# Performance work log

Measured on AMD Instinct MI355X. Metric: run time of the kernel, lower is better.

Reference implementation:

```python
import jax, jax.numpy as jnp
import numpy as np

B, S, D_MODEL, H, D_HEAD = 4, 2048, 1024, 16, 64
SCALE = D_HEAD ** -0.5


def setup_inputs() -> dict:
    key = jax.random.key(0)
    ks = jax.random.split(key, 6)
    init = lambda k, shp: jax.random.normal(k, shp, jnp.float32) * (shp[0] ** -0.5)
    Xq = jax.random.normal(ks[0], (B, S, D_MODEL), jnp.float32)
    # pre-softmax bool mask: True = masked (fill -inf) -> causal
    mask_bef = jnp.triu(jnp.ones((S, S), dtype=bool), k=1)
    # post-softmax bool mask: True = zero out that attention weight
    mask_aft = jax.random.bernoulli(ks[1], 0.1, (S, S))
    Wq = init(ks[2], (D_MODEL, H * D_HEAD))
    Wk = init(ks[3], (D_MODEL, H * D_HEAD))
    Wv = init(ks[4], (D_MODEL, H * D_HEAD))
    Wo = init(ks[5], (H * D_HEAD, D_MODEL))
    return {"Xq": Xq, "mask_bef": mask_bef, "mask_aft": mask_aft,
            "Wq": Wq, "Wk": Wk, "Wv": Wv, "Wo": Wo}


def reference(Xq, mask_bef, mask_aft, Wq, Wk, Wv, Wo):
    # Self-attention: Xk = Xv = Xq
    def split_heads(X, W):  # [B,S,D] @ [D,H*d] -> [B,H,S,d]
        return (X @ W).reshape(B, S, H, D_HEAD).transpose(0, 2, 1, 3)

    Q = split_heads(Xq, Wq)
    K = split_heads(Xq, Wk)
    V = split_heads(Xq, Wv)
    # scores: [B,H,Sq,Sk]
    scores = jnp.einsum('bhqd,bhkd->bhqk', Q, K) * SCALE
    scores = jnp.where(mask_bef, -jnp.inf, scores)  # pre-softmax bool mask
    attn = jax.nn.softmax(scores, axis=-1)
    attn = jnp.where(mask_aft, 0.0, attn)           # post-softmax bool mask
    out = jnp.einsum('bhqk,bhkd->bhqd', attn, V)    # [B,H,S,d]
    out = out.transpose(0, 2, 1, 3).reshape(B, S, H * D_HEAD)
    return out @ Wo  # [B,S,out_dim_o]
```

## Files before the change

### kernel.cpp

```cpp
#include <hip/hip_runtime.h>
#include <hip/hip_bf16.h>


using bf16 = __hip_bfloat16;
typedef __attribute__((ext_vector_type(8))) short short8;
typedef __attribute__((ext_vector_type(4))) float floatx4;

#define kB 4
#define kS 2048
#define kDM 1024
#define kH 16
#define kDH 64
#define kHeadElems ((size_t)kB * kH * kS * kDH)
#define STR 72

__device__ __forceinline__ float bfu(unsigned short v) {
    return __uint_as_float(((unsigned)v) << 16);
}
__device__ __forceinline__ unsigned short f2bf(float f) {
    union { float f; unsigned u; } x{f};
    unsigned r = x.u + 0x7fff + ((x.u >> 16) & 1);
    return (unsigned short)(r >> 16);
}
__device__ __forceinline__ void gl_lds16(const void* g, void* l) {
    __builtin_amdgcn_global_load_lds(
        (const __attribute__((address_space(1))) unsigned int*)g,
        (__attribute__((address_space(3))) unsigned int*)l, 16, 0, 0);
}

__global__ __launch_bounds__(256)
void pack_mask(const int* __restrict__ mask_aft, unsigned long long* __restrict__ mp)
{
    const int widx = blockIdx.x * 4 + (threadIdx.x >> 6);
    const int lane = threadIdx.x & 63;
    const int q = widx >> 5, w64 = widx & 31;
    const int key = w64 * 64 + lane;
    const int m = mask_aft[(size_t)q * kS + key];
    const unsigned long long b = __ballot(m != 0 || key > q);
    if (lane == 0) mp[widx] = b;
}

__global__ __launch_bounds__(256)
void conv_x(const float* __restrict__ X, bf16* __restrict__ Xb)
{
    const size_t i = ((size_t)blockIdx.x * 256 + threadIdx.x) * 8;
    const float4 a = *(const float4*)(X + i);
    const float4 b = *(const float4*)(X + i + 4);
    union { unsigned short u[8]; uint4 v; } o;
    o.u[0] = f2bf(a.x); o.u[1] = f2bf(a.y); o.u[2] = f2bf(a.z); o.u[3] = f2bf(a.w);
    o.u[4] = f2bf(b.x); o.u[5] = f2bf(b.y); o.u[6] = f2bf(b.z); o.u[7] = f2bf(b.w);
    *(uint4*)(Xb + i) = o.v;
}

__global__ __launch_bounds__(256)
void conv_wT(const float* __restrict__ W, bf16* __restrict__ WT)
{
    __shared__ unsigned short Ls[64][STR];
    const int k0 = blockIdx.x * 64, n0 = blockIdx.y * 64;
    const int tid = threadIdx.x;
    const int r16 = tid >> 4, c4 = (tid & 15) * 4;
    #pragma unroll
    for (int it = 0; it < 4; ++it) {
        const int r = it * 16 + r16;
        const float4 v = *(const float4*)(W + (size_t)(k0 + r) * kDM + n0 + c4);
        Ls[c4 + 0][r] = f2bf(v.x); Ls[c4 + 1][r] = f2bf(v.y);
        Ls[c4 + 2][r] = f2bf(v.z); Ls[c4 + 3][r] = f2bf(v.w);
    }
    __syncthreads();
    #pragma unroll
    for (int it = 0; it < 4; ++it) {
        const int rn = it * 16 + r16;
        ushort4 u;
        u.x = Ls[rn][c4 + 0]; u.y = Ls[rn][c4 + 1];
        u.z = Ls[rn][c4 + 2]; u.w = Ls[rn][c4 + 3];
        *(ushort4*)(WT + (size_t)(n0 + rn) * kDM + k0 + c4) = u;
    }
}

__global__ __launch_bounds__(256)
void qkv_mfma(const bf16* __restrict__ A, const bf16* __restrict__ BT,
              bf16* __restrict__ ws)
{
    __shared__ __align__(16) unsigned short At[128][32];
    __shared__ __align__(16) unsigned short Bt[128][32];
    const int tid = threadIdx.x;
    const int w = tid >> 6, lane = tid & 63;
    const int quad = (tid >> 4) & 3, col = tid & 15;
    const int wm = w >> 1, wn = w & 1;
    const int n0 = blockIdx.x * 128;
    const int m0 = blockIdx.y * 128;

    const bf16* pA = A  + (size_t)(m0 + w * 32 + (lane >> 2)) * kDM + (lane & 3) * 8;
    const bf16* pB = BT + (size_t)(n0 + w * 32 + (lane >> 2)) * kDM + (lane & 3) * 8;
    unsigned short* lA = &At[w * 32][0];
    unsigned short* lB = &Bt[w * 32][0];

    floatx4 acc[4][4];
    #pragma unroll
    for (int i = 0; i < 4; ++i)
        #pragma unroll
        for (int j = 0; j < 4; ++j) acc[i][j] = (floatx4){0.f, 0.f, 0.f, 0.f};

    for (int k0 = 0; k0 < kDM; k0 += 32) {
        __syncthreads();
        gl_lds16(pA + k0, lA);
        gl_lds16(pA + k0 + 16 * kDM, lA + 16 * 32);
        gl_lds16(pB + k0, lB);
        gl_lds16(pB + k0 + 16 * kDM, lB + 16 * 32);
        __syncthreads();
        short8 aA[4], bB[4];
        #pragma unroll
        for (int i = 0; i < 4; ++i)
            aA[i] = *(const short8*)&At[wm * 64 + i * 16 + col][quad * 8];
        #pragma unroll
        for (int j = 0; j < 4; ++j)
            bB[j] = *(const short8*)&Bt[wn * 64 + j * 16 + col][quad * 8];
        #pragma unroll
        for (int i = 0; i < 4; ++i)
            #pragma unroll
            for (int j = 0; j < 4; ++j)
                acc[i][j] = __builtin_amdgcn_mfma_f32_16x16x32_bf16(aA[i], bB[j], acc[i][j], 0, 0, 0);
    }

    const int p  = n0 >> 10;
    const int nn = n0 & 1023;
    const float scl = (p == 0) ? 0.125f : 1.0f;
    bf16* Out = ws + (size_t)p * kHeadElems;
    #pragma unroll
    for (int i = 0; i < 4; ++i) {
        #pragma unroll
        for (int r = 0; r < 4; ++r) {
            const int m = m0 + wm * 64 + i * 16 + quad * 4 + r;
            const int b = m >> 11, s = m & 2047;
            #pragma unroll
            for (int j = 0; j < 4; ++j) {
                const int n = nn + wn * 64 + j * 16 + col;
                const int h = n >> 6, d = n & 63;
                Out[((size_t)(b * kH + h) * kS + s) * kDH + d] = __float2bfloat16(acc[i][j][r] * scl);
            }
        }
    }
}

__global__ __launch_bounds__(256)
void vtrans(const bf16* __restrict__ V, bf16* __restrict__ VT)
{
    const int bh = blockIdx.y;
    const int s0 = blockIdx.x * 64;
    const bf16* src = V + (size_t)bh * kS * kDH;
    bf16* dst = VT + (size_t)bh * kS * kDH;
    __shared__ unsigned short L[64][STR];
    const int tid = threadIdx.x;
    #pragma unroll
    for (int t = 0; t < 2; ++t) {
        const int idx = t * 256 + tid;
        const int r = idx >> 3, c8 = (idx & 7) * 8;
        *(uint4*)&L[r][c8] = *(const uint4*)(src + (size_t)(s0 + r) * kDH + c8);
    }
    __syncthreads();
    #pragma unroll
    for (int t = 0; t < 2; ++t) {
        const int idx = t * 256 + tid;
        const int d = idx >> 3, sc = (idx & 7) * 8;
        unsigned short tmp[8];
        #pragma unroll
        for (int e = 0; e < 8; ++e) tmp[e] = L[sc + e][d];
        *(uint4*)(dst + (size_t)d * kS + s0 + sc) = *(uint4*)tmp;
    }
}

__global__ __launch_bounds__(256)
void attn_mfma(const bf16* __restrict__ ws, const bf16* __restrict__ VT,
               const unsigned long long* __restrict__ mp,
               bf16* __restrict__ Aout)
{
    const int bh = blockIdx.y;
    const int b = bh >> 4, h = bh & 15;
    const int qtile = 31 - blockIdx.x;
    const int q0 = qtile * 64;
    const int tid = threadIdx.x;
    const int w    = tid >> 6;
    const int lane = tid & 63;
    const int quad = (tid >> 4) & 3;
    const int col  = tid & 15;

    const size_t ho = (size_t)bh * kS * kDH;
    const bf16* Qg  = ws + ho;
    const bf16* Kg  = ws + kHeadElems + ho;
    const bf16* VTg = VT + ho;

    __shared__ __align__(16) unsigned short Ks[64][64];
    __shared__ __align__(16) unsigned short Vs[64][64];
    __shared__ __align__(16) unsigned short Pw[4][16][STR];
    __shared__ unsigned long long Mw[64];

    const int qw = q0 + w * 16;
    const short8 bQ0 = *(const short8*)(Qg + (size_t)(qw + col) * kDH + quad * 8);
    const short8 bQ1 = *(const short8*)(Qg + (size_t)(qw + col) * kDH + 32 + quad * 8);

    const int swz = col & 7;
    const int sch = (lane & 7) ^ (lane >> 3);

    floatx4 Ov[4] = {{0.f,0.f,0.f,0.f},{0.f,0.f,0.f,0.f},{0.f,0.f,0.f,0.f},{0.f,0.f,0.f,0.f}};
    float lacc = 0.f;

    for (int kt = 0; kt <= qtile; ++kt) {
        __syncthreads();
        #pragma unroll
        for (int t = 0; t < 2; ++t) {
            const int rbase = (t * 4 + w) * 8;
            const int r = rbase + (lane >> 3);
            gl_lds16(Kg  + (size_t)(kt * 64 + r) * kDH + sch * 8, &Ks[rbase][0]);
            gl_lds16(VTg + (size_t)r * kS + kt * 64 + sch * 8,    &Vs[rbase][0]);
        }
        if (tid < 64) Mw[tid] = mp[(size_t)(q0 + tid) * 32 + kt];
        __syncthreads();

        floatx4 sg[4];
        #pragma unroll
        for (int g = 0; g < 4; ++g) {
            const int krow = g * 16 + col;
            const short8 aK0 = *(const short8*)&Ks[krow][(quad ^ swz) * 8];
            const short8 aK1 = *(const short8*)&Ks[krow][((4 + quad) ^ swz) * 8];
            floatx4 s = {0.f, 0.f, 0.f, 0.f};
            s = __builtin_amdgcn_mfma_f32_16x16x32_bf16(aK0, bQ0, s, 0, 0, 0);
            s = __builtin_amdgcn_mfma_f32_16x16x32_bf16(aK1, bQ1, s, 0, 0, 0);
            sg[g] = s;
        }

        const unsigned long long wr = Mw[w * 16 + col] >> (quad * 4);
        const unsigned wlo = (unsigned)wr, whi = (unsigned)(wr >> 32);
        float pv[16];
        if (kt == qtile) {
            #pragma unroll
            for (int g = 0; g < 4; ++g)
                #pragma unroll
                for (int r = 0; r < 4; ++r) {
                    const int key = kt * 64 + g * 16 + quad * 4 + r;
                    const float pe = __expf(sg[g][r]);
                    const float p = (key <= qw + col) ? pe : 0.f;
                    lacc += p;
                    const unsigned wsel = (g < 2) ? wlo : whi;
                    pv[g * 4 + r] = ((wsel >> ((g & 1) * 16 + r)) & 1u) ? 0.f : p;
                }
        } else {
            #pragma unroll
            for (int g = 0; g < 4; ++g)
                #pragma unroll
                for (int r = 0; r < 4; ++r) {
                    const float p = __expf(sg[g][r]);
                    lacc += p;
                    const unsigned wsel = (g < 2) ? wlo : whi;
                    pv[g * 4 + r] = ((wsel >> ((g & 1) * 16 + r)) & 1u) ? 0.f : p;
                }
        }

        #pragma unroll
        for (int g = 0; g < 4; ++g) {
            const unsigned b0 = __float_as_uint(pv[g * 4 + 0]) + 0x8000u;
            const unsigned b1 = __float_as_uint(pv[g * 4 + 1]) + 0x8000u;
            const unsigned b2 = __float_as_uint(pv[g * 4 + 2]) + 0x8000u;
            const unsigned b3 = __float_as_uint(pv[g * 4 + 3]) + 0x8000u;
            uint2 pk;
            pk.x = __builtin_amdgcn_perm(b1, b0, 0x07060302u);
            pk.y = __builtin_amdgcn_perm(b3, b2, 0x07060302u);
            *(uint2*)&Pw[w][col][g * 16 + quad * 4] = pk;
        }

        const short8 aP0 = *(const short8*)&Pw[w][col][quad * 8];
        const short8 aP1 = *(const short8*)&Pw[w][col][32 + quad * 8];
        #pragma unroll
        for (int dg = 0; dg < 4; ++dg) {
            const int vrow = dg * 16 + col;
            const short8 bV0 = *(const short8*)&Vs[vrow][(quad ^ swz) * 8];
            const short8 bV1 = *(const short8*)&Vs[vrow][((4 + quad) ^ swz) * 8];
            Ov[dg] = __builtin_amdgcn_mfma_f32_16x16x32_bf16(aP0, bV0, Ov[dg], 0, 0, 0);
            Ov[dg] = __builtin_amdgcn_mfma_f32_16x16x32_bf16(aP1, bV1, Ov[dg], 0, 0, 0);
        }
    }

    float l = lacc;
    l += __shfl_xor(l, 16, 64);
    l += __shfl_xor(l, 32, 64);
    const float linv = 1.f / l;
    #pragma unroll
    for (int r = 0; r < 4; ++r) {
        const float sc = __shfl(linv, quad * 4 + r, 64);
        const int q = qw + quad * 4 + r;
        bf16* orow = Aout + ((size_t)(b * kS + q)) * kDM + h * kDH;
        #pragma unroll
        for (int dg = 0; dg < 4; ++dg)
            orow[dg * 16 + col] = __float2bfloat16(Ov[dg][r] * sc);
    }
}

__global__ __launch_bounds__(256)
void out_mfma(const bf16* __restrict__ A, const bf16* __restrict__ BT,
              float* __restrict__ Out)
{
    __shared__ __align__(16) unsigned short At[128][32];
    __shared__ __align__(16) unsigned short Bt[128][32];
    const int tid = threadIdx.x;
    const int w = tid >> 6, lane = tid & 63;
    const int quad = (tid >> 4) & 3, col = tid & 15;
    const int wm = w >> 1, wn = w & 1;
    const int n0 = blockIdx.x * 128;
    const int m0 = blockIdx.y * 128;

    const bf16* pA = A  + (size_t)(m0 + w * 32 + (lane >> 2)) * kDM + (lane & 3) * 8;
    const bf16* pB = BT + (size_t)(n0 + w * 32 + (lane >> 2)) * kDM + (lane & 3) * 8;
    unsigned short* lA = &At[w * 32][0];
    unsigned short* lB = &Bt[w * 32][0];

    floatx4 acc[4][4];
    #pragma unroll
    for (int i = 0; i < 4; ++i)
        #pragma unroll
        for (int j = 0; j < 4; ++j) acc[i][j] = (floatx4){0.f, 0.f, 0.f, 0.f};

    for (int k0 = 0; k0 < kDM; k0 += 32) {
        __syncthreads();
        gl_lds16(pA + k0, lA);
        gl_lds16(pA + k0 + 16 * kDM, lA + 16 * 32);
        gl_lds16(pB + k0, lB);
        gl_lds16(pB + k0 + 16 * kDM, lB + 16 * 32);
        __syncthreads();
        short8 aA[4], bB[4];
        #pragma unroll
        for (int i = 0; i < 4; ++i)
            aA[i] = *(const short8*)&At[wm * 64 + i * 16 + col][quad * 8];
        #pragma unroll
        for (int j = 0; j < 4; ++j)
            bB[j] = *(const short8*)&Bt[wn * 64 + j * 16 + col][quad * 8];
        #pragma unroll
        for (int i = 0; i < 4; ++i)
            #pragma unroll
            for (int j = 0; j < 4; ++j)
                acc[i][j] = __builtin_amdgcn_mfma_f32_16x16x32_bf16(aA[i], bB[j], acc[i][j], 0, 0, 0);
    }

    #pragma unroll
    for (int i = 0; i < 4; ++i)
        #pragma unroll
        for (int r = 0; r < 4; ++r) {
            const int m = m0 + wm * 64 + i * 16 + quad * 4 + r;
            #pragma unroll
            for (int j = 0; j < 4; ++j)
                Out[(size_t)m * kDM + n0 + wn * 64 + j * 16 + col] = acc[i][j][r];
        }
}

extern "C" void kernel_launch(void* const* d_in, const int* in_sizes, int n_in,
                              void* d_out, int out_size, void* d_ws, size_t ws_size,
                              hipStream_t stream)
{
    const float* Xq       = (const float*)d_in[0];
    const int*   mask_aft = (const int*)d_in[2];
    const float* Wq       = (const float*)d_in[3];
    const float* Wk       = (const float*)d_in[4];
    const float* Wv       = (const float*)d_in[5];
    const float* Wo       = (const float*)d_in[6];
    float* out = (float*)d_out;

    bf16* ws   = (bf16*)d_ws;
    bf16* Xbf  = ws + 3 * kHeadElems;
    bf16* Aout = Xbf;
    bf16* WoT  = ws;

    unsigned long long* mp = (unsigned long long*)d_out;
    bf16* WcatT = (bf16*)d_out + 262144;
    bf16* VT    = (bf16*)((char*)d_out + 8u * 1024 * 1024);

    pack_mask<<<dim3(kS * 32 / 4), 256, 0, stream>>>(mask_aft, mp);
    conv_x  <<<dim3(4096), 256, 0, stream>>>(Xq, Xbf);
    conv_wT <<<dim3(16, 16), 256, 0, stream>>>(Wq, WcatT);
    conv_wT <<<dim3(16, 16), 256, 0, stream>>>(Wk, WcatT + (size_t)kDM * kDM);
    conv_wT <<<dim3(16, 16), 256, 0, stream>>>(Wv, WcatT + 2 * (size_t)kDM * kDM);
    qkv_mfma<<<dim3(24, 64), 256, 0, stream>>>(Xbf, WcatT, ws);
    vtrans  <<<dim3(32, 64), 256, 0, stream>>>(ws + 2 * kHeadElems, VT);
    attn_mfma<<<dim3(32, 64), 256, 0, stream>>>(ws, VT, mp, Aout);
    conv_wT <<<dim3(16, 16), 256, 0, stream>>>(Wo, WoT);
    out_mfma<<<dim3(8, 64), 256, 0, stream>>>(Aout, WoT, out);
}
```

Before: 354.4 us.

## Restructure attention: 128-row query tiles, direct global K/V loads, expanded bf16 mask

The attention kernel now has each block cover 128 query rows, with each wave handling two 16-row subtiles so every K/V fragment feeds twice as many MFMAs. K and V are read straight from global memory instead of being staged through LDS with barriers, and blocks are remapped so each XCD gets a group of heads with balanced causal q-tile ordering. The post-softmax mask is pre-expanded into a 16-bit AND mask (0 or 0xFFFF per key) and applied to the packed bf16 probabilities. The softmax uses exp2, with log2(e) folded into the Q scale. This trades the LDS reuse and coalesced staging of K/V for fewer syncs and higher MFMA density, and it adds an 8MB mask read in place of the bit-packed mask.

Result: slower. 454.9 us (+28.4%).

```diff
diff --git a/kernel.cpp b/kernel.cpp
--- a/kernel.cpp
+++ b/kernel.cpp
@@ -14,9 +14,12 @@
 #define kHeadElems ((size_t)kB * kH * kS * kDH)
 #define STR 72
 
-__device__ __forceinline__ float bfu(unsigned short v) {
-    return __uint_as_float(((unsigned)v) << 16);
-}
+#if __has_builtin(__builtin_amdgcn_exp2f)
+#define EXP2(x) __builtin_amdgcn_exp2f(x)
+#else
+#define EXP2(x) __expf((x) * 0.69314718056f)
+#endif
+
 __device__ __forceinline__ unsigned short f2bf(float f) {
     union { float f; unsigned u; } x{f};
     unsigned r = x.u + 0x7fff + ((x.u >> 16) & 1);
@@ -29,15 +32,23 @@
 }
 
 __global__ __launch_bounds__(256)
-void pack_mask(const int* __restrict__ mask_aft, unsigned long long* __restrict__ mp)
-{
-    const int widx = blockIdx.x * 4 + (threadIdx.x >> 6);
-    const int lane = threadIdx.x & 63;
-    const int q = widx >> 5, w64 = widx & 31;
-    const int key = w64 * 64 + lane;
-    const int m = mask_aft[(size_t)q * kS + key];
-    const unsigned long long b = __ballot(m != 0 || key > q);
-    if (lane == 0) mp[widx] = b;
+void pack_em(const int* __restrict__ mask_aft, unsigned short* __restrict__ EM)
+{
+    const size_t i = ((size_t)blockIdx.x * 256 + threadIdx.x) * 8;
+    const int q  = (int)(i >> 11);
+    const int k0 = (int)(i & 2047);
+    const int4 m0 = *(const int4*)(mask_aft + i);
+    const int4 m1 = *(const int4*)(mask_aft + i + 4);
+    union { unsigned short u[8]; uint4 v; } o;
+    o.u[0] = (m0.x || (k0 + 0) > q) ? 0 : 0xFFFFu;
+    o.u[1] = (m0.y || (k0 + 1) > q) ? 0 : 0xFFFFu;
+    o.u[2] = (m0.z || (k0 + 2) > q) ? 0 : 0xFFFFu;
+    o.u[3] = (m0.w || (k0 + 3) > q) ? 0 : 0xFFFFu;
+    o.u[4] = (m1.x || (k0 + 4) > q) ? 0 : 0xFFFFu;
+    o.u[5] = (m1.y || (k0 + 5) > q) ? 0 : 0xFFFFu;
+    o.u[6] = (m1.z || (k0 + 6) > q) ? 0 : 0xFFFFu;
+    o.u[7] = (m1.w || (k0 + 7) > q) ? 0 : 0xFFFFu;
+    *(uint4*)(EM + i) = o.v;
 }
 
 __global__ __launch_bounds__(256)
@@ -124,7 +135,7 @@
 
     const int p  = n0 >> 10;
     const int nn = n0 & 1023;
-    const float scl = (p == 0) ? 0.125f : 1.0f;
+    const float scl = (p == 0) ? 0.18033688f : 1.0f;
     bf16* Out = ws + (size_t)p * kHeadElems;
     #pragma unroll
     for (int i = 0; i < 4; ++i) {
@@ -171,16 +182,20 @@
 
 __global__ __launch_bounds__(256)
 void attn_mfma(const bf16* __restrict__ ws, const bf16* __restrict__ VT,
-               const unsigned long long* __restrict__ mp,
+               const unsigned short* __restrict__ EM,
                bf16* __restrict__ Aout)
 {
-    const int bh = blockIdx.y;
+    const int flat = blockIdx.x + blockIdx.y * 16;
+    const int xcd = flat & 7;
+    const int idx = flat >> 3;
+    const int bh  = xcd * 8 + (idx & 7);
+    const int j   = idx >> 3;
+    const int qtile = (j & 1) ? (j >> 1) : (15 - (j >> 1));
+    const int q0 = qtile * 128;
+
     const int b = bh >> 4, h = bh & 15;
-    const int qtile = 31 - blockIdx.x;
-    const int q0 = qtile * 64;
-    const int tid = threadIdx.x;
+    const int tid  = threadIdx.x;
     const int w    = tid >> 6;
-    const int lane = tid & 63;
     const int quad = (tid >> 4) & 3;
     const int col  = tid & 15;
 
@@ -189,108 +204,114 @@
     const bf16* Kg  = ws + kHeadElems + ho;
     const bf16* VTg = VT + ho;
 
-    __shared__ __align__(16) unsigned short Ks[64][64];
-    __shared__ __align__(16) unsigned short Vs[64][64];
-    __shared__ __align__(16) unsigned short Pw[4][16][STR];
-    __shared__ unsigned long long Mw[64];
-
-    const int qw = q0 + w * 16;
-    const short8 bQ0 = *(const short8*)(Qg + (size_t)(qw + col) * kDH + quad * 8);
-    const short8 bQ1 = *(const short8*)(Qg + (size_t)(qw + col) * kDH + 32 + quad * 8);
-
-    const int swz = col & 7;
-    const int sch = (lane & 7) ^ (lane >> 3);
-
-    floatx4 Ov[4] = {{0.f,0.f,0.f,0.f},{0.f,0.f,0.f,0.f},{0.f,0.f,0.f,0.f},{0.f,0.f,0.f,0.f}};
-    float lacc = 0.f;
-
-    for (int kt = 0; kt <= qtile; ++kt) {
-        __syncthreads();
-        #pragma unroll
-        for (int t = 0; t < 2; ++t) {
-            const int rbase = (t * 4 + w) * 8;
-            const int r = rbase + (lane >> 3);
-            gl_lds16(Kg  + (size_t)(kt * 64 + r) * kDH + sch * 8, &Ks[rbase][0]);
-            gl_lds16(VTg + (size_t)r * kS + kt * 64 + sch * 8,    &Vs[rbase][0]);
-        }
-        if (tid < 64) Mw[tid] = mp[(size_t)(q0 + tid) * 32 + kt];
-        __syncthreads();
-
-        floatx4 sg[4];
+    __shared__ __align__(16) unsigned short Pw[4][2][16][STR];
+
+    const int qw = q0 + w * 32;
+
+    short8 bQ[2][2];
+    const unsigned short* EMq[2];
+    #pragma unroll
+    for (int sub = 0; sub < 2; ++sub) {
+        const bf16* qrow = Qg + (size_t)(qw + sub * 16 + col) * kDH;
+        bQ[sub][0] = *(const short8*)(qrow + quad * 8);
+        bQ[sub][1] = *(const short8*)(qrow + 32 + quad * 8);
+        EMq[sub] = EM + (size_t)(qw + sub * 16 + col) * kS;
+    }
+
+    floatx4 Ov[2][4];
+    #pragma unroll
+    for (int sub = 0; sub < 2; ++sub)
+        #pragma unroll
+        for (int dg = 0; dg < 4; ++dg) Ov[sub][dg] = (floatx4){0.f, 0.f, 0.f, 0.f};
+    float lacc[2] = {0.f, 0.f};
+
+    const int ktmax = (qw + 31) >> 6;
+    for (int kt = 0; kt <= ktmax; ++kt) {
+        const int kt64 = kt * 64;
+        const bf16* Kt = Kg  + (size_t)kt64 * kDH;
+        const bf16* Vt = VTg + kt64;
+
+        floatx4 sg[2][4];
         #pragma unroll
         for (int g = 0; g < 4; ++g) {
-            const int krow = g * 16 + col;
-            const short8 aK0 = *(const short8*)&Ks[krow][(quad ^ swz) * 8];
-            const short8 aK1 = *(const short8*)&Ks[krow][((4 + quad) ^ swz) * 8];
-            floatx4 s = {0.f, 0.f, 0.f, 0.f};
-            s = __builtin_amdgcn_mfma_f32_16x16x32_bf16(aK0, bQ0, s, 0, 0, 0);
-            s = __builtin_amdgcn_mfma_f32_16x16x32_bf16(aK1, bQ1, s, 0, 0, 0);
-            sg[g] = s;
-        }
-
-        const unsigned long long wr = Mw[w * 16 + col] >> (quad * 4);
-        const unsigned wlo = (unsigned)wr, whi = (unsigned)(wr >> 32);
-        float pv[16];
-        if (kt == qtile) {
-            #pragma unroll
-            for (int g = 0; g < 4; ++g)
-                #pragma unroll
-                for (int r = 0; r < 4; ++r) {
-                    const int key = kt * 64 + g * 16 + quad * 4 + r;
-                    const float pe = __expf(sg[g][r]);
-                    const float p = (key <= qw + col) ? pe : 0.f;
-                    lacc += p;
-                    const unsigned wsel = (g < 2) ? wlo : whi;
-                    pv[g * 4 + r] = ((wsel >> ((g & 1) * 16 + r)) & 1u) ? 0.f : p;
+            const bf16* krow = Kt + (size_t)(g * 16 + col) * kDH;
+            const short8 aK0 = *(const short8*)(krow + quad * 8);
+            const short8 aK1 = *(const short8*)(krow + 32 + quad * 8);
+            floatx4 sA = {0.f, 0.f, 0.f, 0.f}, sB = {0.f, 0.f, 0.f, 0.f};
+            sA = __builtin_amdgcn_mfma_f32_16x16x32_bf16(aK0, bQ[0][0], sA, 0, 0, 0);
+            sA = __builtin_amdgcn_mfma_f32_16x16x32_bf16(aK1, bQ[0][1], sA, 0, 0, 0);
+            sB = __builtin_amdgcn_mfma_f32_16x16x32_bf16(aK0, bQ[1][0], sB, 0, 0, 0);
+            sB = __builtin_amdgcn_mfma_f32_16x16x32_bf16(aK1, bQ[1][1], sB, 0, 0, 0);
+            sg[0][g] = sA; sg[1][g] = sB;
+        }
+
+        #pragma unroll
+        for (int sub = 0; sub < 2; ++sub) {
+            const int qbase = qw + sub * 16;
+            const bool needC = (kt64 + 63 > qbase);
+            float lc = 0.f;
+            #pragma unroll
+            for (int g = 0; g < 4; ++g) {
+                const float p0 = EXP2(sg[sub][g][0]);
+                const float p1 = EXP2(sg[sub][g][1]);
+                const float p2 = EXP2(sg[sub][g][2]);
+                const float p3 = EXP2(sg[sub][g][3]);
+                if (needC) {
+                    const int kb = kt64 + g * 16 + quad * 4;
+                    const int qme = qbase + col;
+                    lc += (kb + 0 <= qme) ? p0 : 0.f;
+                    lc += (kb + 1 <= qme) ? p1 : 0.f;
+                    lc += (kb + 2 <= qme) ? p2 : 0.f;
+                    lc += (kb + 3 <= qme) ? p3 : 0.f;
+                } else {
+                    lc += (p0 + p1) + (p2 + p3);
                 }
-        } else {
-            #pragma unroll
-            for (int g = 0; g < 4; ++g)
-                #pragma unroll
-                for (int r = 0; r < 4; ++r) {
-                    const float p = __expf(sg[g][r]);
-                    lacc += p;
-                    const unsigned wsel = (g < 2) ? wlo : whi;
-                    pv[g * 4 + r] = ((wsel >> ((g & 1) * 16 + r)) & 1u) ? 0.f : p;
-                }
-        }
-
-        #pragma unroll
-        for (int g = 0; g < 4; ++g) {
-            const unsigned b0 = __float_as_uint(pv[g * 4 + 0]) + 0x8000u;
-            const unsigned b1 = __float_as_uint(pv[g * 4 + 1]) + 0x8000u;
-            const unsigned b2 = __float_as_uint(pv[g * 4 + 2]) + 0x8000u;
-            const unsigned b3 = __float_as_uint(pv[g * 4 + 3]) + 0x8000u;
-            uint2 pk;
-            pk.x = __builtin_amdgcn_perm(b1, b0, 0x07060302u);
-            pk.y = __builtin_amdgcn_perm(b3, b2, 0x07060302u);
-            *(uint2*)&Pw[w][col][g * 16 + quad * 4] = pk;
-        }
-
-        const short8 aP0 = *(const short8*)&Pw[w][col][quad * 8];
-        const short8 aP1 = *(const short8*)&Pw[w][col][32 + quad * 8];
+                const unsigned b0 = __float_as_uint(p0) + 0x8000u;
+                const unsigned b1 = __float_as_uint(p1) + 0x8000u;
+                const unsigned b2 = __float_as_uint(p2) + 0x8000u;
+                const unsigned b3 = __float_as_uint(p3) + 0x8000u;
+                uint2 pk;
+                pk.x = __builtin_amdgcn_perm(b1, b0, 0x07060302u);
+                pk.y = __builtin_amdgcn_perm(b3, b2, 0x07060302u);
+                const uint2 em = *(const uint2*)(EMq[sub] + kt64 + g * 16 + quad * 4);
+                pk.x &= em.x; pk.y &= em.y;
+                *(uint2*)&Pw[w][sub][col][g * 16 + quad * 4] = pk;
+            }
+            lacc[sub] += lc;
+        }
+
+        const short8 aP[2][2] = {
+            { *(const short8*)&Pw[w][0][col][quad * 8],
+              *(const short8*)&Pw[w][0][col][32 + quad * 8] },
+            { *(const short8*)&Pw[w][1][col][quad * 8],
+              *(const short8*)&Pw[w][1][col][32 + quad * 8] } };
         #pragma unroll
         for (int dg = 0; dg < 4; ++dg) {
-            const int vrow = dg * 16 + col;
-            const short8 bV0 = *(const short8*)&Vs[vrow][(quad ^ swz) * 8];
-            const short8 bV1 = *(const short8*)&Vs[vrow][((4 + quad) ^ swz) * 8];
-            Ov[dg] = __builtin_amdgcn_mfma_f32_16x16x32_bf16(aP0, bV0, Ov[dg], 0, 0, 0);
-            Ov[dg] = __builtin_amdgcn_mfma_f32_16x16x32_bf16(aP1, bV1, Ov[dg], 0, 0, 0);
-        }
-    }
-
-    float l = lacc;
-    l += __shfl_xor(l, 16, 64);
-    l += __shfl_xor(l, 32, 64);
-    const float linv = 1.f / l;
-    #pragma unroll
-    for (int r = 0; r < 4; ++r) {
-        const float sc = __shfl(linv, quad * 4 + r, 64);
-        const int q = qw + quad * 4 + r;
-        bf16* orow = Aout + ((size_t)(b * kS + q)) * kDM + h * kDH;
-        #pragma unroll
-        for (int dg = 0; dg < 4; ++dg)
-            orow[dg * 16 + col] = __float2bfloat16(Ov[dg][r] * sc);
+            const bf16* vrow = Vt + (size_t)(dg * 16 + col) * kS;
+            const short8 bV0 = *(const short8*)(vrow + quad * 8);
+            const short8 bV1 = *(const short8*)(vrow + 32 + quad * 8);
+            Ov[0][dg] = __builtin_amdgcn_mfma_f32_16x16x32_bf16(aP[0][0], bV0, Ov[0][dg], 0, 0, 0);
+            Ov[0][dg] = __builtin_amdgcn_mfma_f32_16x16x32_bf16(aP[0][1], bV1, Ov[0][dg], 0, 0, 0);
+            Ov[1][dg] = __builtin_amdgcn_mfma_f32_16x16x32_bf16(aP[1][0], bV0, Ov[1][dg], 0, 0, 0);
+            Ov[1][dg] = __builtin_amdgcn_mfma_f32_16x16x32_bf16(aP[1][1], bV1, Ov[1][dg], 0, 0, 0);
+        }
+    }
+
+    #pragma unroll
+    for (int sub = 0; sub < 2; ++sub) {
+        float l = lacc[sub];
+        l += __shfl_xor(l, 16, 64);
+        l += __shfl_xor(l, 32, 64);
+        const float linv = 1.f / l;
+        #pragma unroll
+        for (int r = 0; r < 4; ++r) {
+            const float sc = __shfl(linv, quad * 4 + r, 64);
+            const int q = qw + sub * 16 + quad * 4 + r;
+            bf16* orow = Aout + ((size_t)(b * kS + q)) * kDM + h * kDH;
+            #pragma unroll
+            for (int dg = 0; dg < 4; ++dg)
+                orow[dg * 16 + col] = __float2bfloat16(Ov[sub][dg][r] * sc);
+        }
     }
 }
 
@@ -367,18 +388,18 @@
     bf16* Aout = Xbf;
     bf16* WoT  = ws;
 
-    unsigned long long* mp = (unsigned long long*)d_out;
     bf16* WcatT = (bf16*)d_out + 262144;
     bf16* VT    = (bf16*)((char*)d_out + 8u * 1024 * 1024);
-
-    pack_mask<<<dim3(kS * 32 / 4), 256, 0, stream>>>(mask_aft, mp);
+    unsigned short* EMp = (unsigned short*)((char*)d_out + 24u * 1024 * 1024);
+
+    pack_em <<<dim3(2048), 256, 0, stream>>>(mask_aft, EMp);
     conv_x  <<<dim3(4096), 256, 0, stream>>>(Xq, Xbf);
     conv_wT <<<dim3(16, 16), 256, 0, stream>>>(Wq, WcatT);
     conv_wT <<<dim3(16, 16), 256, 0, stream>>>(Wk, WcatT + (size_t)kDM * kDM);
     conv_wT <<<dim3(16, 16), 256, 0, stream>>>(Wv, WcatT + 2 * (size_t)kDM * kDM);
     qkv_mfma<<<dim3(24, 64), 256, 0, stream>>>(Xbf, WcatT, ws);
     vtrans  <<<dim3(32, 64), 256, 0, stream>>>(ws + 2 * kHeadElems, VT);
-    attn_mfma<<<dim3(32, 64), 256, 0, stream>>>(ws, VT, mp, Aout);
+    attn_mfma<<<dim3(16, 64), 256, 0, stream>>>(ws, VT, EMp, Aout);
     conv_wT <<<dim3(16, 16), 256, 0, stream>>>(Wo, WoT);
     out_mfma<<<dim3(8, 64), 256, 0, stream>>>(Aout, WoT, out);
 }
```
